# Kernel tuning notes

Measured on AMD Instinct MI355X. Metric: run time of the kernel, lower is better.

Reference implementation:

```python
import jax, jax.numpy as jnp
import numpy as np

B, N, Q, D, H = 8, 2048, 256, 1024, 16
HD = D // H


def setup_inputs() -> dict:
    key = jax.random.key(0)
    ks = jax.random.split(key, 6)
    scale = 1.0 / np.sqrt(D)
    return {
        "sources": jax.random.normal(ks[0], (B, N, D), dtype=jnp.float32),
        "queries": jax.random.normal(ks[1], (B, Q, D), dtype=jnp.float32),
        "w_in": jax.random.normal(ks[2], (3 * D, D), dtype=jnp.float32) * scale,
        "b_in": jax.random.normal(ks[3], (3 * D,), dtype=jnp.float32) * 0.02,
        "w_out": jax.random.normal(ks[4], (D, D), dtype=jnp.float32) * scale,
        "b_out": jax.random.normal(ks[5], (D,), dtype=jnp.float32) * 0.02,
    }


def reference(sources, queries, w_in, b_in, w_out, b_out):
    # torch nn.MultiheadAttention (batch_first, eval mode, no attn_mask),
    # applied per-sample with equal lengths == one batched cross-attention.
    w_q, w_k, w_v = jnp.split(w_in, 3, axis=0)   # each [D, D]
    b_q, b_k, b_v = jnp.split(b_in, 3, axis=0)
    q = queries @ w_q.T + b_q                    # [B, Q, D]
    k = sources @ w_k.T + b_k                    # [B, N, D]
    v = sources @ w_v.T + b_v                    # [B, N, D]
    q = q.reshape(B, Q, H, HD)
    k = k.reshape(B, N, H, HD)
    v = v.reshape(B, N, H, HD)
    scale = 1.0 / np.sqrt(HD).astype(np.float32)
    scores = jnp.einsum("bqhd,bkhd->bhqk", q, k) * scale  # [B, H, Q, N]
    attn = jax.nn.softmax(scores, axis=-1)
    out = jnp.einsum("bhqk,bkhd->bqhd", attn, v).reshape(B, Q, D)
    out = out @ w_out.T + b_out                  # out_proj
    return out + queries                         # residual (fix=False: no norm)
```

## Files before the change

### kernel.cpp

```cpp
#include <hip/hip_runtime.h>
#include <hip/hip_bf16.h>


typedef unsigned short u16;
typedef __attribute__((ext_vector_type(8))) short short8;
typedef __attribute__((ext_vector_type(4))) float floatx4;

static_assert(sizeof(short8) == 16, "short8 must be 16B");

__device__ __forceinline__ u16 f2bf(float f) {
  unsigned int x = __float_as_uint(f);
  x += 0x7fffu + ((x >> 16) & 1u);
  return (u16)(x >> 16);
}

__device__ __forceinline__ void gload16(const u16* g, u16* lds) {
  __builtin_amdgcn_global_load_lds(
      (const __attribute__((address_space(1))) unsigned int*)g,
      (__attribute__((address_space(3))) unsigned int*)lds, 16, 0, 0);
}

template <int N> __device__ __forceinline__ void vmwait() {
  if constexpr (N == 0)      asm volatile("s_waitcnt vmcnt(0)" ::: "memory");
  else if constexpr (N == 4) asm volatile("s_waitcnt vmcnt(4)" ::: "memory");
  else if constexpr (N == 6) asm volatile("s_waitcnt vmcnt(6)" ::: "memory");
  else if constexpr (N == 8) asm volatile("s_waitcnt vmcnt(8)" ::: "memory");
  else static_assert(N == 0, "unsupported vmcnt immediate");
}

__device__ __forceinline__ void sfence() { __builtin_amdgcn_sched_barrier(0); }

__global__ __launch_bounds__(256) void f2bf_multi(
    const float* __restrict__ s, u16* __restrict__ so,
    const float* __restrict__ q, u16* __restrict__ qo,
    const float* __restrict__ wi, u16* __restrict__ wio,
    const float* __restrict__ wo, u16* __restrict__ woo) {
  int i = blockIdx.x * 256 + threadIdx.x;
  const float* in; u16* out; int idx;
  if (i < 4194304)      { in = s;  out = so;  idx = i; }
  else if (i < 4718592) { in = q;  out = qo;  idx = i - 4194304; }
  else if (i < 5505024) { in = wi; out = wio; idx = i - 4718592; }
  else if (i < 5767168) { in = wo; out = woo; idx = i - 5505024; }
  else return;
  float4 v = reinterpret_cast<const float4*>(in)[idx];
  ushort4 o;
  o.x = f2bf(v.x); o.y = f2bf(v.y); o.z = f2bf(v.z); o.w = f2bf(v.w);
  reinterpret_cast<ushort4*>(out)[idx] = o;
}

template <int MT, int NT>
__device__ __forceinline__ void gemm_core(
    const u16* __restrict__ A, int lda,
    const u16* __restrict__ Bm, int ldb, int K,
    u16* __restrict__ Alds, u16* __restrict__ Blds,
    floatx4 (&acc)[MT][NT]) {
  const int t = threadIdx.x;
  const int wave = t >> 6, lane = t & 63;
  const int rr = lane & 15, kq = lane >> 4;
  constexpr int AI = MT, BI = NT;
  constexpr int AELEMS = MT * 32 * 64;
  constexpr int BELEMS = NT * 32 * 64;

  const u16* ag[AI]; u16* al[AI];
#pragma unroll
  for (int i = 0; i < AI; ++i) {
    int s = i * 256 + t;
    int row = s >> 3, c16 = s & 7;
    ag[i] = A + (size_t)row * lda + ((c16 ^ (row & 7)) * 8);
    al[i] = Alds + (size_t)(i * 256 + wave * 64) * 8;
  }
  const u16* bg[BI]; u16* blp[BI];
#pragma unroll
  for (int i = 0; i < BI; ++i) {
    int s = i * 256 + t;
    int row = s >> 3, c16 = s & 7;
    bg[i] = Bm + (size_t)row * ldb + ((c16 ^ (row & 7)) * 8);
    blp[i] = Blds + (size_t)(i * 256 + wave * 64) * 8;
  }

  const int m0w = (wave & 1) * (MT * 16);
  const int n0w = (wave >> 1) * (NT * 16);
  int aoff[MT][2], boff[NT][2];
#pragma unroll
  for (int mi = 0; mi < MT; ++mi) {
    int row = m0w + mi * 16 + rr;
#pragma unroll
    for (int kk = 0; kk < 2; ++kk)
      aoff[mi][kk] = row * 64 + (((kk * 4 + kq) ^ (row & 7)) * 8);
  }
#pragma unroll
  for (int ni = 0; ni < NT; ++ni) {
    int row = n0w + ni * 16 + rr;
#pragma unroll
    for (int kk = 0; kk < 2; ++kk)
      boff[ni][kk] = row * 64 + (((kk * 4 + kq) ^ (row & 7)) * 8);
  }

  auto compute = [&](int bs) {
    const u16* Ab = Alds + bs * AELEMS;
    const u16* Bb = Blds + bs * BELEMS;
#pragma unroll
    for (int kk = 0; kk < 2; ++kk) {
      short8 af[MT], bfr[NT];
#pragma unroll
      for (int mi = 0; mi < MT; ++mi)
        af[mi] = *reinterpret_cast<const short8*>(Ab + aoff[mi][kk]);
#pragma unroll
      for (int ni = 0; ni < NT; ++ni)
        bfr[ni] = *reinterpret_cast<const short8*>(Bb + boff[ni][kk]);
      __builtin_amdgcn_s_setprio(1);
#pragma unroll
      for (int mi = 0; mi < MT; ++mi)
#pragma unroll
        for (int ni = 0; ni < NT; ++ni)
          acc[mi][ni] = __builtin_amdgcn_mfma_f32_16x16x32_bf16(af[mi], bfr[ni], acc[mi][ni], 0, 0, 0);
      __builtin_amdgcn_s_setprio(0);
    }
  };

  const int nt = K >> 6;

#pragma unroll
  for (int i = 0; i < AI; ++i) gload16(ag[i], al[i]);
#pragma unroll
  for (int i = 0; i < BI; ++i) gload16(bg[i], blp[i]);

  int cur = 0;
#pragma unroll 1
  for (int tt = 0; tt < nt - 1; ++tt) {
    const int nxt = cur ^ 1;
    const int koff = (tt + 1) * 64;
#pragma unroll
    for (int i = 0; i < AI; ++i) gload16(ag[i] + koff, al[i] + nxt * AELEMS);
#pragma unroll
    for (int i = 0; i < BI; ++i) gload16(bg[i] + koff, blp[i] + nxt * BELEMS);
    sfence();
    vmwait<AI + BI>();
    __builtin_amdgcn_s_barrier();
    sfence();
    compute(cur);
    sfence();
    __builtin_amdgcn_s_barrier();
    cur = nxt;
  }
  sfence();
  vmwait<0>();
  __builtin_amdgcn_s_barrier();
  sfence();
  compute(cur);
}

__global__ __launch_bounds__(256, 2) void gemm_proj(
    const u16* __restrict__ s_bf, const u16* __restrict__ qy_bf,
    const u16* __restrict__ wi_bf, const float* __restrict__ b_in,
    u16* __restrict__ kp, u16* __restrict__ vT, u16* __restrict__ qp) {
  __shared__ __attribute__((aligned(16))) u16 Alds[2 * 128 * 64];
  __shared__ __attribute__((aligned(16))) u16 Blds[2 * 128 * 64];
  const int by = blockIdx.y, bx = blockIdx.x;
  const bool isq = (by >= 128);
  if (isq && bx >= 8) return;
  const int mB = (isq ? by - 128 : by) * 128;
  const int nB = bx * 128;
  const u16* A = (isq ? qy_bf : s_bf) + (size_t)mB * 1024;
  const u16* W = wi_bf + (size_t)(isq ? nB : 1024 + nB) * 1024;
  const float* bias = b_in + (isq ? nB : 1024 + nB);

  const floatx4 zz = {0.f, 0.f, 0.f, 0.f};
  floatx4 acc[4][4] = {{zz, zz, zz, zz}, {zz, zz, zz, zz}, {zz, zz, zz, zz}, {zz, zz, zz, zz}};
  gemm_core<4, 4>(A, 1024, W, 1024, 1024, Alds, Blds, acc);

  const int lane = threadIdx.x & 63, wave = threadIdx.x >> 6;
  const int rr = lane & 15, r4 = (lane >> 4) * 4;
  const int m0w = (wave & 1) * 64, n0w = (wave >> 1) * 64;

  if (isq) {
#pragma unroll
    for (int mi = 0; mi < 4; ++mi)
#pragma unroll
      for (int ni = 0; ni < 4; ++ni) {
        int nl = n0w + ni * 16 + rr;
        float bv = bias[nl];
#pragma unroll
        for (int r = 0; r < 4; ++r) {
          int m = mB + m0w + mi * 16 + r4 + r;
          qp[(size_t)m * 1024 + nB + nl] = f2bf((acc[mi][ni][r] + bv) * 0.125f);
        }
      }
  } else if (nB < 1024) {
#pragma unroll
    for (int mi = 0; mi < 4; ++mi)
#pragma unroll
      for (int ni = 0; ni < 4; ++ni) {
        int nl = n0w + ni * 16 + rr;
        float bv = bias[nl];
#pragma unroll
        for (int r = 0; r < 4; ++r) {
          int m = mB + m0w + mi * 16 + r4 + r;
          kp[(size_t)m * 1024 + nB + nl] = f2bf(acc[mi][ni][r] + bv);
        }
      }
  } else {
#pragma unroll
    for (int mi = 0; mi < 4; ++mi)
#pragma unroll
      for (int ni = 0; ni < 4; ++ni) {
        int n2 = nB + n0w + ni * 16 + rr - 1024;
        int h = n2 >> 6, d = n2 & 63;
        float bv = bias[n0w + ni * 16 + rr];
        int m0 = mB + m0w + mi * 16 + r4;
        int b = m0 >> 11, j0 = m0 & 2047;
        ushort4 o;
        o.x = f2bf(acc[mi][ni][0] + bv);
        o.y = f2bf(acc[mi][ni][1] + bv);
        o.z = f2bf(acc[mi][ni][2] + bv);
        o.w = f2bf(acc[mi][ni][3] + bv);
        *reinterpret_cast<ushort4*>(
            vT + ((size_t)(b * 16 + h) * 64 + d) * 2048 + j0) = o;
      }
  }
}

__global__ __launch_bounds__(256, 2) void gemm_scores_exp(
    const u16* __restrict__ qp, const u16* __restrict__ kp,
    u16* __restrict__ sc, int b0) {
  __shared__ __attribute__((aligned(16))) u16 Alds[128 * 64];
  __shared__ __attribute__((aligned(16))) u16 Blds[128 * 64];
  const int bz = blockIdx.z, bl = bz >> 4, h = bz & 15;
  const int b = b0 + bl;
  const int mB = blockIdx.y * 128;
  const int nB = blockIdx.x * 128;
  const u16* A = qp + (size_t)b * 256 * 1024 + h * 64 + (size_t)mB * 1024;
  const u16* Bm = kp + (size_t)b * 2048 * 1024 + h * 64 + (size_t)nB * 1024;
  u16* C = sc + (size_t)bz * 256 * 2048;
  const floatx4 zz = {0.f, 0.f, 0.f, 0.f};
  floatx4 acc[4][4] = {{zz, zz, zz, zz}, {zz, zz, zz, zz}, {zz, zz, zz, zz}, {zz, zz, zz, zz}};
  gemm_core<4, 4>(A, 1024, Bm, 1024, 64, Alds, Blds, acc);

  const int lane = threadIdx.x & 63, wave = threadIdx.x >> 6;
  const int rr = lane & 15, r4 = (lane >> 4) * 4;
  const int m0w = (wave & 1) * 64, n0w = (wave >> 1) * 64;
#pragma unroll
  for (int mi = 0; mi < 4; ++mi)
#pragma unroll
    for (int ni = 0; ni < 4; ++ni) {
      int n = nB + n0w + ni * 16 + rr;
#pragma unroll
      for (int r = 0; r < 4; ++r) {
        int m = mB + m0w + mi * 16 + r4 + r;
        C[(size_t)m * 2048 + n] = f2bf(__expf(acc[mi][ni][r]));
      }
    }
}

__global__ __launch_bounds__(256, 2) void gemm_pv(
    const u16* __restrict__ sc, const u16* __restrict__ vT,
    u16* __restrict__ ao, int b0) {
  __shared__ __attribute__((aligned(16))) u16 Alds[2 * 64 * 64];
  __shared__ __attribute__((aligned(16))) u16 Blds[2 * 64 * 64];
  const int t = threadIdx.x;
  const int wave = t >> 6, lane = t & 63;
  const int rr = lane & 15, kq = lane >> 4;
  const int bz = blockIdx.z, bl = bz >> 4, h = bz & 15;
  const int b = b0 + bl;
  const int mB = blockIdx.y * 64;
  const u16* A = sc + (size_t)bz * 256 * 2048 + (size_t)mB * 2048;
  const u16* Bm = vT + (size_t)(b * 16 + h) * 64 * 2048;

  const u16* ag[2]; u16* al[2]; const u16* bg[2]; u16* blp[2];
#pragma unroll
  for (int i = 0; i < 2; ++i) {
    int s = i * 256 + t, row = s >> 3, c16 = s & 7;
    ag[i] = A + (size_t)row * 2048 + ((c16 ^ (row & 7)) * 8);
    al[i] = Alds + (size_t)(i * 256 + wave * 64) * 8;
    bg[i] = Bm + (size_t)row * 2048 + ((c16 ^ (row & 7)) * 8);
    blp[i] = Blds + (size_t)(i * 256 + wave * 64) * 8;
  }

  const int m0w = (wave & 1) * 32;
  const int n0w = (wave >> 1) * 32;
  int aoff[2][2], boff[2][2];
#pragma unroll
  for (int mi = 0; mi < 2; ++mi) {
    int row = m0w + mi * 16 + rr;
#pragma unroll
    for (int kk = 0; kk < 2; ++kk)
      aoff[mi][kk] = row * 64 + (((kk * 4 + kq) ^ (row & 7)) * 8);
  }
#pragma unroll
  for (int ni = 0; ni < 2; ++ni) {
    int row = n0w + ni * 16 + rr;
#pragma unroll
    for (int kk = 0; kk < 2; ++kk)
      boff[ni][kk] = row * 64 + (((kk * 4 + kq) ^ (row & 7)) * 8);
  }

  const short ov = (rr == 0) ? (short)0x3F80 : (short)0;
  const short8 ones = {ov, ov, ov, ov, ov, ov, ov, ov};

  const floatx4 zz = {0.f, 0.f, 0.f, 0.f};
  floatx4 acc[2][2] = {{zz, zz}, {zz, zz}};
  floatx4 acc_l[2] = {zz, zz};

  auto compute = [&](int bs) {
    const u16* Ab = Alds + bs * 4096;
    const u16* Bb = Blds + bs * 4096;
#pragma unroll
    for (int kk = 0; kk < 2; ++kk) {
      short8 af[2], bfr[2];
#pragma unroll
      for (int mi = 0; mi < 2; ++mi)
        af[mi] = *reinterpret_cast<const short8*>(Ab + aoff[mi][kk]);
#pragma unroll
      for (int ni = 0; ni < 2; ++ni)
        bfr[ni] = *reinterpret_cast<const short8*>(Bb + boff[ni][kk]);
      __builtin_amdgcn_s_setprio(1);
#pragma unroll
      for (int mi = 0; mi < 2; ++mi) {
#pragma unroll
        for (int ni = 0; ni < 2; ++ni)
          acc[mi][ni] = __builtin_amdgcn_mfma_f32_16x16x32_bf16(af[mi], bfr[ni], acc[mi][ni], 0, 0, 0);
        acc_l[mi] = __builtin_amdgcn_mfma_f32_16x16x32_bf16(af[mi], ones, acc_l[mi], 0, 0, 0);
      }
      __builtin_amdgcn_s_setprio(0);
    }
  };

#pragma unroll
  for (int i = 0; i < 2; ++i) gload16(ag[i], al[i]);
#pragma unroll
  for (int i = 0; i < 2; ++i) gload16(bg[i], blp[i]);

  int cur = 0;
#pragma unroll 1
  for (int tt = 0; tt < 31; ++tt) {
    const int nxt = cur ^ 1;
    const int koff = (tt + 1) * 64;
#pragma unroll
    for (int i = 0; i < 2; ++i) gload16(ag[i] + koff, al[i] + nxt * 4096);
#pragma unroll
    for (int i = 0; i < 2; ++i) gload16(bg[i] + koff, blp[i] + nxt * 4096);
    sfence();
    vmwait<4>();
    __builtin_amdgcn_s_barrier();
    sfence();
    compute(cur);
    sfence();
    __builtin_amdgcn_s_barrier();
    cur = nxt;
  }
  sfence();
  vmwait<0>();
  __builtin_amdgcn_s_barrier();
  sfence();
  compute(cur);

#pragma unroll
  for (int mi = 0; mi < 2; ++mi)
#pragma unroll
    for (int r = 0; r < 4; ++r) {
      float l = __shfl(acc_l[mi][r], lane & 48, 64);
      float inv = 1.0f / l;
      int m = mB + m0w + mi * 16 + kq * 4 + r;
#pragma unroll
      for (int ni = 0; ni < 2; ++ni) {
        int n = n0w + ni * 16 + rr;
        ao[(size_t)(b * 256 + m) * 1024 + h * 64 + n] = f2bf(acc[mi][ni][r] * inv);
      }
    }
}

__global__ __launch_bounds__(256, 2) void gemm_out(
    const u16* __restrict__ A, const u16* __restrict__ W,
    const float* __restrict__ bias, const float* __restrict__ resid,
    float* __restrict__ out) {
  __shared__ __attribute__((aligned(16))) u16 Alds[2 * 64 * 64];
  __shared__ __attribute__((aligned(16))) u16 Blds[2 * 128 * 64];
  const int mB = blockIdx.y * 64;
  const int nB = blockIdx.x * 128;
  const floatx4 zz = {0.f, 0.f, 0.f, 0.f};
  floatx4 acc[2][4] = {{zz, zz, zz, zz}, {zz, zz, zz, zz}};
  gemm_core<2, 4>(A + (size_t)mB * 1024, 1024, W + (size_t)nB * 1024, 1024, 1024,
                  Alds, Blds, acc);
  const int lane = threadIdx.x & 63, wave = threadIdx.x >> 6;
  const int rr = lane & 15, r4 = (lane >> 4) * 4;
  const int m0w = (wave & 1) * 32, n0w = (wave >> 1) * 64;
#pragma unroll
  for (int mi = 0; mi < 2; ++mi)
#pragma unroll
    for (int ni = 0; ni < 4; ++ni) {
      int n = nB + n0w + ni * 16 + rr;
      float bv = bias[n];
#pragma unroll
      for (int r = 0; r < 4; ++r) {
        int m = mB + m0w + mi * 16 + r4 + r;
        size_t idx = (size_t)m * 1024 + n;
        out[idx] = acc[mi][ni][r] + bv + resid[idx];
      }
    }
}

extern "C" void kernel_launch(void* const* d_in, const int* in_sizes, int n_in,
                              void* d_out, int out_size, void* d_ws, size_t ws_size,
                              hipStream_t stream) {
  const float* sources = (const float*)d_in[0];
  const float* queries = (const float*)d_in[1];
  const float* w_in    = (const float*)d_in[2];
  const float* b_in    = (const float*)d_in[3];
  const float* w_out   = (const float*)d_in[4];
  const float* b_out   = (const float*)d_in[5];
  float* out = (float*)d_out;

  char* ws = (char*)d_ws;
  size_t off = 0;
  auto alloc = [&](size_t elems) -> u16* {
    u16* p = (u16*)(ws + off);
    off += elems * sizeof(u16);
    off = (off + 255) & ~(size_t)255;
    return p;
  };
  u16* s_bf  = alloc((size_t)16777216);
  u16* qy_bf = alloc((size_t)2097152);
  u16* wi_bf = alloc((size_t)3145728);
  u16* wo_bf = alloc((size_t)1048576);
  u16* qp    = alloc((size_t)2097152);
  u16* kp    = alloc((size_t)16777216);
  u16* vT    = alloc((size_t)16777216);
  u16* ao    = alloc((size_t)2097152);
  const size_t sc_elems_per_b = (size_t)16 * 256 * 2048;
  size_t remain = ws_size > off ? ws_size - off : 0;
  int bchunk = (int)(remain / (sc_elems_per_b * sizeof(u16)));
  if (bchunk > 8) bchunk = 8;
  if (bchunk < 1) bchunk = 1;
  u16* sc = (u16*)(ws + off);

  f2bf_multi<<<dim3(22528), 256, 0, stream>>>(
      sources, s_bf, queries, qy_bf, w_in, wi_bf, w_out, wo_bf);

  gemm_proj<<<dim3(16, 144), 256, 0, stream>>>(
      s_bf, qy_bf, wi_bf, b_in, kp, vT, qp);

  for (int b0 = 0; b0 < 8; b0 += bchunk) {
    int nb = (8 - b0) < bchunk ? (8 - b0) : bchunk;
    gemm_scores_exp<<<dim3(16, 2, nb * 16), 256, 0, stream>>>(qp, kp, sc, b0);
    gemm_pv<<<dim3(1, 4, nb * 16), 256, 0, stream>>>(sc, vT, ao, b0);
  }

  gemm_out<<<dim3(8, 32), 256, 0, stream>>>(ao, wo_bf, b_out, queries, out);
}
```

Before: 309.9 us.

## Split KV projection into 256x256-tile 8-wave pipelined GEMM with block swizzle

Result: no change. 314.6 us (+1.5%).

```diff
diff --git a/kernel.cpp b/kernel.cpp
--- a/kernel.cpp
+++ b/kernel.cpp
@@ -26,6 +26,10 @@
   else if constexpr (N == 6) asm volatile("s_waitcnt vmcnt(6)" ::: "memory");
   else if constexpr (N == 8) asm volatile("s_waitcnt vmcnt(8)" ::: "memory");
   else static_assert(N == 0, "unsupported vmcnt immediate");
+}
+
+__device__ __forceinline__ void lgkm0() {
+  asm volatile("s_waitcnt lgkmcnt(0)" ::: "memory");
 }
 
 __device__ __forceinline__ void sfence() { __builtin_amdgcn_sched_barrier(0); }
@@ -150,45 +154,149 @@
   compute(cur);
 }
 
-__global__ __launch_bounds__(256, 2) void gemm_proj(
-    const u16* __restrict__ s_bf, const u16* __restrict__ qy_bf,
-    const u16* __restrict__ wi_bf, const float* __restrict__ b_in,
-    u16* __restrict__ kp, u16* __restrict__ vT, u16* __restrict__ qp) {
-  __shared__ __attribute__((aligned(16))) u16 Alds[2 * 128 * 64];
-  __shared__ __attribute__((aligned(16))) u16 Blds[2 * 128 * 64];
-  const int by = blockIdx.y, bx = blockIdx.x;
-  const bool isq = (by >= 128);
-  if (isq && bx >= 8) return;
-  const int mB = (isq ? by - 128 : by) * 128;
-  const int nB = bx * 128;
-  const u16* A = (isq ? qy_bf : s_bf) + (size_t)mB * 1024;
-  const u16* W = wi_bf + (size_t)(isq ? nB : 1024 + nB) * 1024;
-  const float* bias = b_in + (isq ? nB : 1024 + nB);
-
+
+template <int LO>
+__device__ __forceinline__ void read_a8(const u16* ab, int kcol0, int kcol1,
+                                        short8 (&af)[8][2]) {
+#pragma unroll
+  for (int mi = 0; mi < 4; ++mi) {
+    af[LO + mi][0] = *reinterpret_cast<const short8*>(ab + (LO + mi) * 1024 + kcol0);
+    af[LO + mi][1] = *reinterpret_cast<const short8*>(ab + (LO + mi) * 1024 + kcol1);
+  }
+}
+
+template <int LO>
+__device__ __forceinline__ void read_b8(const u16* bb, int kcol0, int kcol1,
+                                        short8 (&bf)[4][2]) {
+#pragma unroll
+  for (int ni = 0; ni < 2; ++ni) {
+    bf[LO + ni][0] = *reinterpret_cast<const short8*>(bb + (LO + ni) * 1024 + kcol0);
+    bf[LO + ni][1] = *reinterpret_cast<const short8*>(bb + (LO + ni) * 1024 + kcol1);
+  }
+}
+
+template <int M0, int N0>
+__device__ __forceinline__ void quad8(const short8 (&af)[8][2], const short8 (&bf)[4][2],
+                                      floatx4 (&acc)[8][4]) {
+  __builtin_amdgcn_s_setprio(1);
+#pragma unroll
+  for (int kk = 0; kk < 2; ++kk)
+#pragma unroll
+    for (int mi = 0; mi < 4; ++mi)
+#pragma unroll
+      for (int ni = 0; ni < 2; ++ni)
+        acc[M0 + mi][N0 + ni] = __builtin_amdgcn_mfma_f32_16x16x32_bf16(
+            af[M0 + mi][kk], bf[N0 + ni][kk], acc[M0 + mi][N0 + ni], 0, 0, 0);
+  __builtin_amdgcn_s_setprio(0);
+}
+
+__global__ __launch_bounds__(512, 2) void gemm_proj_kv8(
+    const u16* __restrict__ s_bf, const u16* __restrict__ wi_bf,
+    const float* __restrict__ b_in,
+    u16* __restrict__ kp, u16* __restrict__ vT) {
+  __shared__ __attribute__((aligned(16))) u16 Alds[2 * 256 * 64];
+  __shared__ __attribute__((aligned(16))) u16 Blds[2 * 256 * 64];
+
+  int bid = blockIdx.y * 8 + blockIdx.x;
+  int nb = (bid & 7) * 64 + (bid >> 3);
+  const int by = nb >> 3, bx = nb & 7;
+  const int mB = by * 256;
+  const int nB = bx * 256;
+  const u16* Ag = s_bf + (size_t)mB * 1024;
+  const u16* Wg = wi_bf + (size_t)(1024 + nB) * 1024;
+  const float* bias = b_in + 1024 + nB;
+
+  const int t = threadIdx.x;
+  const int w = t >> 6, lane = t & 63;
+  const int rr = lane & 15, kq = lane >> 4;
+  const int wr = w >> 2, wc = w & 3;
+
+  const u16* ga[2][2]; const u16* gb[2][2];
+#pragma unroll
+  for (int h = 0; h < 2; ++h)
+#pragma unroll
+    for (int i = 0; i < 2; ++i) {
+      int s = i * 512 + t;
+      int row = h * 128 + (s >> 3), c16 = s & 7;
+      ga[h][i] = Ag + (size_t)row * 1024 + ((c16 ^ (row & 7)) * 8);
+      gb[h][i] = Wg + (size_t)row * 1024 + ((c16 ^ (row & 7)) * 8);
+    }
+
+#define STAGE_A8(j, h) { const int d_ = ((j) & 1) * 16384;                         \
+    gload16(ga[h][0] + (size_t)(j) * 64, Alds + d_ + (h) * 8192 + w * 512);        \
+    gload16(ga[h][1] + (size_t)(j) * 64, Alds + d_ + (h) * 8192 + 4096 + w * 512); }
+#define STAGE_B8(j, h) { const int d_ = ((j) & 1) * 16384;                         \
+    gload16(gb[h][0] + (size_t)(j) * 64, Blds + d_ + (h) * 8192 + w * 512);        \
+    gload16(gb[h][1] + (size_t)(j) * 64, Blds + d_ + (h) * 8192 + 4096 + w * 512); }
+
+  const int kcol0 = ((kq) ^ (rr & 7)) * 8;
+  const int kcol1 = ((4 + kq) ^ (rr & 7)) * 8;
+  const u16* abase = Alds + (wr * 128 + rr) * 64;
+  const u16* bbase = Blds + (wc * 64 + rr) * 64;
+
+  short8 af[8][2], bf[4][2];
   const floatx4 zz = {0.f, 0.f, 0.f, 0.f};
-  floatx4 acc[4][4] = {{zz, zz, zz, zz}, {zz, zz, zz, zz}, {zz, zz, zz, zz}, {zz, zz, zz, zz}};
-  gemm_core<4, 4>(A, 1024, W, 1024, 1024, Alds, Blds, acc);
-
-  const int lane = threadIdx.x & 63, wave = threadIdx.x >> 6;
-  const int rr = lane & 15, r4 = (lane >> 4) * 4;
-  const int m0w = (wave & 1) * 64, n0w = (wave >> 1) * 64;
-
-  if (isq) {
-#pragma unroll
-    for (int mi = 0; mi < 4; ++mi)
-#pragma unroll
-      for (int ni = 0; ni < 4; ++ni) {
-        int nl = n0w + ni * 16 + rr;
-        float bv = bias[nl];
-#pragma unroll
-        for (int r = 0; r < 4; ++r) {
-          int m = mB + m0w + mi * 16 + r4 + r;
-          qp[(size_t)m * 1024 + nB + nl] = f2bf((acc[mi][ni][r] + bv) * 0.125f);
-        }
-      }
-  } else if (nB < 1024) {
-#pragma unroll
-    for (int mi = 0; mi < 4; ++mi)
+  floatx4 acc[8][4];
+#pragma unroll
+  for (int mi = 0; mi < 8; ++mi)
+#pragma unroll
+    for (int ni = 0; ni < 4; ++ni) acc[mi][ni] = zz;
+
+  STAGE_A8(0, 0); STAGE_B8(0, 0); STAGE_A8(0, 1); STAGE_B8(0, 1);
+  STAGE_A8(1, 0); STAGE_B8(1, 0);
+  sfence();
+  vmwait<4>();
+  __builtin_amdgcn_s_barrier();
+  sfence();
+
+#pragma unroll 1
+  for (int kt = 0; kt < 16; ++kt) {
+    const int doff = (kt & 1) * 16384;
+    const u16* ab = abase + doff;
+    const u16* bb = bbase + doff;
+    read_a8<0>(ab, kcol0, kcol1, af);
+    read_b8<0>(bb, kcol0, kcol1, bf);
+    if (kt + 1 < 16) STAGE_A8(kt + 1, 1);
+    sfence();
+    __builtin_amdgcn_s_barrier();
+    lgkm0(); sfence();
+    quad8<0, 0>(af, bf, acc);
+    sfence();
+    __builtin_amdgcn_s_barrier();
+    sfence();
+    read_a8<4>(ab, kcol0, kcol1, af);
+    read_b8<2>(bb, kcol0, kcol1, bf);
+    if (kt + 1 < 16) STAGE_B8(kt + 1, 1);
+    sfence();
+    __builtin_amdgcn_s_barrier();
+    lgkm0(); sfence();
+    quad8<0, 2>(af, bf, acc);
+    sfence();
+    __builtin_amdgcn_s_barrier();
+    sfence();
+    if (kt + 2 < 16) STAGE_A8(kt + 2, 0);
+    sfence();
+    __builtin_amdgcn_s_barrier();
+    quad8<4, 0>(af, bf, acc);
+    sfence();
+    __builtin_amdgcn_s_barrier();
+    sfence();
+    if (kt + 2 < 16) { STAGE_B8(kt + 2, 0); sfence(); vmwait<4>(); }
+    else             { sfence(); vmwait<0>(); }
+    __builtin_amdgcn_s_barrier();
+    quad8<4, 2>(af, bf, acc);
+    sfence();
+    __builtin_amdgcn_s_barrier();
+    sfence();
+  }
+#undef STAGE_A8
+#undef STAGE_B8
+
+  const int r4 = kq * 4;
+  const int m0w = wr * 128, n0w = wc * 64;
+  if (nB < 1024) {
+#pragma unroll
+    for (int mi = 0; mi < 8; ++mi)
 #pragma unroll
       for (int ni = 0; ni < 4; ++ni) {
         int nl = n0w + ni * 16 + rr;
@@ -201,7 +309,7 @@
       }
   } else {
 #pragma unroll
-    for (int mi = 0; mi < 4; ++mi)
+    for (int mi = 0; mi < 8; ++mi)
 #pragma unroll
       for (int ni = 0; ni < 4; ++ni) {
         int n2 = nB + n0w + ni * 16 + rr - 1024;
@@ -218,6 +326,38 @@
             vT + ((size_t)(b * 16 + h) * 64 + d) * 2048 + j0) = o;
       }
   }
+}
+
+__global__ __launch_bounds__(256, 2) void gemm_proj_q(
+    const u16* __restrict__ qy_bf, const u16* __restrict__ wi_bf,
+    const float* __restrict__ b_in, u16* __restrict__ qp) {
+  __shared__ __attribute__((aligned(16))) u16 Alds[2 * 128 * 64];
+  __shared__ __attribute__((aligned(16))) u16 Blds[2 * 128 * 64];
+  const int mB = blockIdx.y * 128;
+  const int nB = blockIdx.x * 128;
+  const u16* A = qy_bf + (size_t)mB * 1024;
+  const u16* W = wi_bf + (size_t)nB * 1024;
+  const float* bias = b_in + nB;
+
+  const floatx4 zz = {0.f, 0.f, 0.f, 0.f};
+  floatx4 acc[4][4] = {{zz, zz, zz, zz}, {zz, zz, zz, zz}, {zz, zz, zz, zz}, {zz, zz, zz, zz}};
+  gemm_core<4, 4>(A, 1024, W, 1024, 1024, Alds, Blds, acc);
+
+  const int lane = threadIdx.x & 63, wave = threadIdx.x >> 6;
+  const int rr = lane & 15, r4 = (lane >> 4) * 4;
+  const int m0w = (wave & 1) * 64, n0w = (wave >> 1) * 64;
+#pragma unroll
+  for (int mi = 0; mi < 4; ++mi)
+#pragma unroll
+    for (int ni = 0; ni < 4; ++ni) {
+      int nl = n0w + ni * 16 + rr;
+      float bv = bias[nl];
+#pragma unroll
+      for (int r = 0; r < 4; ++r) {
+        int m = mB + m0w + mi * 16 + r4 + r;
+        qp[(size_t)m * 1024 + nB + nl] = f2bf((acc[mi][ni][r] + bv) * 0.125f);
+      }
+    }
 }
 
 __global__ __launch_bounds__(256, 2) void gemm_scores_exp(
@@ -436,8 +576,8 @@
   f2bf_multi<<<dim3(22528), 256, 0, stream>>>(
       sources, s_bf, queries, qy_bf, w_in, wi_bf, w_out, wo_bf);
 
-  gemm_proj<<<dim3(16, 144), 256, 0, stream>>>(
-      s_bf, qy_bf, wi_bf, b_in, kp, vT, qp);
+  gemm_proj_kv8<<<dim3(8, 64), 512, 0, stream>>>(s_bf, wi_bf, b_in, kp, vT);
+  gemm_proj_q<<<dim3(8, 16), 256, 0, stream>>>(qy_bf, wi_bf, b_in, qp);
 
   for (int b0 = 0; b0 < 8; b0 += bchunk) {
     int nb = (8 - b0) < bchunk ? (8 - b0) : bchunk;
```
